# Kernel tuning notes

Measured on AMD Instinct MI355X. Metric: run time of the kernel, lower is better.

Reference implementation:

```python
import jax, jax.numpy as jnp
import numpy as np

B, T, S = 64, 128, 512
E, H = 256, 512
GRU_IN = E + 2 * H  # 1280


def setup_inputs() -> dict:
    key = jax.random.key(0)
    ks = jax.random.split(key, 12)
    sc = 0.02
    return {
        "trg_embed": jax.random.normal(ks[0], (B, T, E), jnp.float32),
        "enc_hidden": jax.random.normal(ks[1], (B, S, 2 * H), jnp.float32),
        "enc_final": jax.random.normal(ks[2], (1, B, 2 * H), jnp.float32),
        "data_mask": jnp.ones((B, 1, S), jnp.int32),
        # attention params
        "W_key": jax.random.normal(ks[3], (H, 2 * H), jnp.float32) * sc,
        "W_query": jax.random.normal(ks[4], (H, H), jnp.float32) * sc,
        "w_energy": jax.random.normal(ks[5], (H,), jnp.float32) * sc,
        # bridge
        "W_bridge": jax.random.normal(ks[6], (H, 2 * H), jnp.float32) * sc,
        "b_bridge": jnp.zeros((H,), jnp.float32),
        # GRU (single layer, batch_first)
        "W_ih": jax.random.normal(ks[7], (3 * H, GRU_IN), jnp.float32) * sc,
        "W_hh": jax.random.normal(ks[8], (3 * H, H), jnp.float32) * sc,
        "b_ih": jnp.zeros((3 * H,), jnp.float32),
        "b_hh": jnp.zeros((3 * H,), jnp.float32),
        # pre_out: Linear(H + 2H + E -> H, bias=False)
        "W_pre": jax.random.normal(ks[9], (H, H + 2 * H + E), jnp.float32) * sc,
    }


def _decode(trg_embed, enc_hidden, enc_final, data_mask,
            W_key, W_query, w_energy, W_bridge, b_bridge,
            W_ih, W_hh, b_ih, b_hh, W_pre):
    # bridge: initial hidden state [B, H]
    h0 = jnp.tanh(enc_final[0] @ W_bridge.T + b_bridge)
    # precompute attention keys [B, S, H]
    proj_key = jnp.einsum('bsk,hk->bsh', enc_hidden, W_key)
    mask = data_mask[:, 0, :] != 0  # [B, S]

    def step(h, x_t):  # h: [B,H], x_t: [B,E]
        # Bahdanau attention
        q = x_t_query = h @ W_query.T                      # [B, H]
        e = jnp.einsum('bsh,h->bs', jnp.tanh(q[:, None, :] + proj_key), w_energy)  # [B,S]
        e = jnp.where(mask, e, -1e9)
        alphas = jax.nn.softmax(e, axis=-1)                # [B, S]
        context = jnp.einsum('bs,bsd->bd', alphas, enc_hidden)  # [B, 2H]
        # GRU cell
        x = jnp.concatenate([x_t, context], axis=-1)       # [B, E+2H]
        gx = x @ W_ih.T + b_ih                             # [B, 3H]
        gh = h @ W_hh.T + b_hh                             # [B, 3H]
        rx, zx, nx = jnp.split(gx, 3, axis=-1)
        rh, zh, nh = jnp.split(gh, 3, axis=-1)
        r = jax.nn.sigmoid(rx + rh)
        z = jax.nn.sigmoid(zx + zh)
        n = jnp.tanh(nx + r * nh)
        h_new = (1.0 - z) * n + z * h                      # [B, H]
        # pre-output projection
        pre = jnp.concatenate([x_t, h_new, context], axis=-1) @ W_pre.T  # [B, H]
        return h_new, (h_new, pre)

    xs = jnp.transpose(trg_embed, (1, 0, 2))  # [T, B, E]
    h_last, (states, pre_outs) = jax.lax.scan(step, h0, xs)
    decoder_states = jnp.transpose(states, (1, 0, 2))      # [B, T, H]
    pre_output_vectors = jnp.transpose(pre_outs, (1, 0, 2))  # [B, T, H]
    hidden = h_last[None]                                  # [1, B, H]
    return decoder_states, hidden, pre_output_vectors


def reference(trg_embed, enc_hidden, enc_final, data_mask,
              W_key, W_query, w_energy, W_bridge, b_bridge,
              W_ih, W_hh, b_ih, b_hh, W_pre):
    return _decode(trg_embed, enc_hidden, enc_final, data_mask,
                   W_key, W_query, w_energy, W_bridge, b_bridge,
                   W_ih, W_hh, b_ih, b_hh, W_pre)
```

## Files before the change

kernel.cpp:

```cpp
#include <hip/hip_runtime.h>


#define LDSS 40

typedef short bf16x8 __attribute__((ext_vector_type(8)));
typedef float f32x4 __attribute__((ext_vector_type(4)));

__device__ inline ushort f2b(float f) {
    unsigned int u = __float_as_uint(f);
    return (ushort)((u + 0x7FFFu + ((u >> 16) & 1u)) >> 16);
}
__device__ inline float b2f(ushort u) {
    return __uint_as_float(((unsigned int)u) << 16);
}
__device__ inline float fast_tanh(float x) {
    x = fminf(fmaxf(x, -15.f), 15.f);
    float ex = __expf(2.f * x);
    return (ex - 1.f) / (ex + 1.f);
}

__global__ void f2b4_kernel(const float4* __restrict__ in, ushort4* __restrict__ out, int n4) {
    int i = blockIdx.x * blockDim.x + threadIdx.x;
    int stride = gridDim.x * blockDim.x;
    for (; i < n4; i += stride) {
        float4 v = in[i];
        ushort4 o;
        o.x = f2b(v.x); o.y = f2b(v.y); o.z = f2b(v.z); o.w = f2b(v.w);
        out[i] = o;
    }
}

template <bool AF32, bool ATOMIC>
__device__ inline void gemm64x64(const void* __restrict__ Av,
                                 const ushort* __restrict__ B,
                                 ushort* As, ushort* Bs,
                                 int lda, int ldb, int kbeg, int kend,
                                 float* Cf, ushort* Cb, long ldc,
                                 long m0, long n0)
{
    const int tid  = threadIdx.x;
    const int wave = tid >> 6;
    const int lane = tid & 63;
    const int row  = tid >> 2;
    const int kcol = (tid & 3) * 8;
    const int lrow = lane & 15;
    const int quad = lane >> 4;

    f32x4 acc[4];
#pragma unroll
    for (int i = 0; i < 4; i++) acc[i] = f32x4{0.f, 0.f, 0.f, 0.f};

    const ushort* Ab  = (const ushort*)Av + (m0 + row) * (long)lda + kcol;
    const float*  Afp = (const float*)Av + (m0 + row) * (long)lda + kcol;
    const ushort* Bp  = B + (n0 + row) * (long)ldb + kcol;
    ushort* AsW = As + row * LDSS + kcol;
    ushort* BsW = Bs + row * LDSS + kcol;
    const ushort* AsR = As + (wave * 16 + lrow) * LDSS + quad * 8;
    const ushort* BsR = Bs + lrow * LDSS + quad * 8;

    for (int k0 = kbeg; k0 < kend; k0 += 32) {
        uint4 av;
        if (AF32) {
            float4 f0 = *(const float4*)(Afp + k0);
            float4 f1 = *(const float4*)(Afp + k0 + 4);
            av.x = (uint)f2b(f0.x) | ((uint)f2b(f0.y) << 16);
            av.y = (uint)f2b(f0.z) | ((uint)f2b(f0.w) << 16);
            av.z = (uint)f2b(f1.x) | ((uint)f2b(f1.y) << 16);
            av.w = (uint)f2b(f1.z) | ((uint)f2b(f1.w) << 16);
        } else {
            av = *(const uint4*)(Ab + k0);
        }
        uint4 bv = *(const uint4*)(Bp + k0);
        __syncthreads();
        *(uint4*)AsW = av;
        *(uint4*)BsW = bv;
        __syncthreads();
        bf16x8 af = *(const bf16x8*)AsR;
#pragma unroll
        for (int nf = 0; nf < 4; nf++) {
            bf16x8 bfv = *(const bf16x8*)(BsR + nf * 16 * LDSS);
            acc[nf] = __builtin_amdgcn_mfma_f32_16x16x32_bf16(af, bfv, acc[nf], 0, 0, 0);
        }
    }

#pragma unroll
    for (int nf = 0; nf < 4; nf++) {
#pragma unroll
        for (int r = 0; r < 4; r++) {
            long m = m0 + wave * 16 + quad * 4 + r;
            long n = n0 + nf * 16 + lrow;
            float v = acc[nf][r];
            if (ATOMIC)      atomicAdd(&Cf[m * ldc + n], v);
            else if (Cf)     Cf[m * ldc + n] = v;
            else             Cb[m * ldc + n] = f2b(v);
        }
    }
}

template <bool AF32>
__global__ void gemm_nt(const void* __restrict__ A, const ushort* __restrict__ B,
                        float* Cf, ushort* Cb,
                        int lda, int ldb, long ldc, int K, int nTilesN)
{
    __shared__ ushort As[64 * LDSS];
    __shared__ ushort Bs[64 * LDSS];
    long m0 = (long)(blockIdx.x / nTilesN) * 64;
    long n0 = (long)(blockIdx.x % nTilesN) * 64;
    gemm64x64<AF32, false>(A, B, As, Bs, lda, ldb, 0, K, Cf, Cb, ldc, m0, n0);
}

__global__ void q_kernel(const ushort* __restrict__ h_b, const ushort* __restrict__ Wq,
                         float* q)
{
    __shared__ ushort As[64 * LDSS];
    __shared__ ushort Bs[64 * LDSS];
    int kc = blockIdx.x >> 3, nt = blockIdx.x & 7;
    gemm64x64<false, true>(h_b, Wq, As, Bs, 512, 512, kc * 256, kc * 256 + 256,
                           q, nullptr, 512, 0, (long)nt * 64);
}

__global__ void gxgh_kernel(const ushort* __restrict__ xcat, const ushort* __restrict__ h_b,
                            const ushort* __restrict__ cat2r,
                            const ushort* __restrict__ Wih, const ushort* __restrict__ Whh,
                            const ushort* __restrict__ Wpre,
                            float* gx, float* gh, float* pre_out, int t)
{
    __shared__ ushort As[64 * LDSS];
    __shared__ ushort Bs[64 * LDSS];
    int bid = blockIdx.x;
    if (bid < 32) {
        if (t == 0) return;
        int kc = bid >> 3, nt = bid & 7;
        gemm64x64<false, true>(cat2r, Wpre, As, Bs, 1792, 1792, kc * 448, kc * 448 + 448,
                               pre_out + (long)(t - 1) * 512, nullptr, 65536, 0, (long)nt * 64);
    } else if (bid < 80) {
        int b3 = bid - 32, kc = b3 / 24, nt = b3 % 24;
        gemm64x64<false, true>(h_b, Whh, As, Bs, 512, 512, kc * 256, kc * 256 + 256,
                               gh, nullptr, 1536, 0, (long)nt * 64);
    } else {
        int b4 = bid - 80, nt = b4 % 24, kc = b4 / 24;
        gemm64x64<false, true>(xcat, Wih, As, Bs, 1280, 1280, kc * 320, kc * 320 + 320,
                               gx, nullptr, 1536, 0, (long)nt * 64);
    }
}

__global__ void e_kernel(const ushort* __restrict__ pk, const float* __restrict__ q,
                         const float* __restrict__ wE, const int* __restrict__ mask,
                         float* __restrict__ e)
{
    int wid  = (blockIdx.x * blockDim.x + threadIdx.x) >> 6;
    int lane = threadIdx.x & 63;
    int b  = wid >> 7;
    int s0 = (wid & 127) << 2;
    const float* qp = q + ((long)b << 9) + lane * 8;
    const float* wp = wE + lane * 8;
    float4 q0 = *(const float4*)qp, q1 = *(const float4*)(qp + 4);
    float4 w0 = *(const float4*)wp, w1 = *(const float4*)(wp + 4);
    const ushort* pkb = pk + (((long)(b << 9) + s0) << 9) + lane * 8;
    bf16x8 pv = *(const bf16x8*)pkb;
#pragma unroll
    for (int j = 0; j < 4; j++) {
        bf16x8 pn;
        if (j < 3) pn = *(const bf16x8*)(pkb + ((long)(j + 1) << 9));
        float acc;
        acc  = fast_tanh(q0.x + b2f((ushort)pv[0])) * w0.x;
        acc += fast_tanh(q0.y + b2f((ushort)pv[1])) * w0.y;
        acc += fast_tanh(q0.z + b2f((ushort)pv[2])) * w0.z;
        acc += fast_tanh(q0.w + b2f((ushort)pv[3])) * w0.w;
        acc += fast_tanh(q1.x + b2f((ushort)pv[4])) * w1.x;
        acc += fast_tanh(q1.y + b2f((ushort)pv[5])) * w1.y;
        acc += fast_tanh(q1.z + b2f((ushort)pv[6])) * w1.z;
        acc += fast_tanh(q1.w + b2f((ushort)pv[7])) * w1.w;
#pragma unroll
        for (int off = 32; off; off >>= 1) acc += __shfl_xor(acc, off);
        if (lane == 0) {
            int i = (b << 9) + s0 + j;
            e[i] = (mask[i] != 0) ? acc : -1e9f;
        }
        pv = pn;
    }
}

__global__ void sc_kernel(const float* __restrict__ e,
                          const float* __restrict__ encf, const ushort* __restrict__ encb,
                          int useb, const float* __restrict__ trg,
                          ushort* __restrict__ xcat, ushort* __restrict__ cat2, int t)
{
    __shared__ float alpha[512];
    __shared__ float red[256];
    __shared__ float part[256];
    int b  = blockIdx.x >> 4;
    int dc = blockIdx.x & 15;
    int tid = threadIdx.x;
    float p0 = __expf(e[(b << 9) + tid]);
    float p1 = __expf(e[(b << 9) + 256 + tid]);
    alpha[tid] = p0;
    alpha[tid + 256] = p1;
    red[tid] = p0 + p1;
    __syncthreads();
    for (int off = 128; off; off >>= 1) {
        if (tid < off) red[tid] += red[tid + off];
        __syncthreads();
    }
    float inv = 1.f / red[0];
    int dl = tid & 63;
    int sr = tid >> 6;
    int d  = (dc << 6) + dl;
    float a0 = 0.f, a1 = 0.f, a2 = 0.f, a3 = 0.f;
    if (useb) {
        const ushort* p = encb + ((long)b << 19) + d;
        for (int s = sr; s < 512; s += 16) {
            a0 += alpha[s]      * b2f(p[(long)s << 10]);
            a1 += alpha[s + 4]  * b2f(p[(long)(s + 4) << 10]);
            a2 += alpha[s + 8]  * b2f(p[(long)(s + 8) << 10]);
            a3 += alpha[s + 12] * b2f(p[(long)(s + 12) << 10]);
        }
    } else {
        const float* p = encf + ((long)b << 19) + d;
        for (int s = sr; s < 512; s += 16) {
            a0 += alpha[s]      * p[(long)s << 10];
            a1 += alpha[s + 4]  * p[(long)(s + 4) << 10];
            a2 += alpha[s + 8]  * p[(long)(s + 8) << 10];
            a3 += alpha[s + 12] * p[(long)(s + 12) << 10];
        }
    }
    part[tid] = ((a0 + a1) + (a2 + a3));
    __syncthreads();
    if (sr == 0) {
        float ctx = (part[dl] + part[64 + dl] + part[128 + dl] + part[192 + dl]) * inv;
        ushort cb = f2b(ctx);
        xcat[b * 1280 + 256 + d] = cb;
        cat2[b * 1792 + 768 + d] = cb;
    } else if (sr == 1 && dc < 4) {
        ushort xv = f2b(trg[((long)b * 128 + t) * 256 + (dc << 6) + dl]);
        xcat[b * 1280 + (dc << 6) + dl] = xv;
        cat2[b * 1792 + (dc << 6) + dl] = xv;
    }
}

__global__ void gates_kernel(float* __restrict__ gx, float* __restrict__ gh,
                             const float* __restrict__ bih, const float* __restrict__ bhh,
                             float* __restrict__ h, ushort* __restrict__ h_b,
                             ushort* __restrict__ cat2, float* __restrict__ d_states,
                             float* __restrict__ q, float* __restrict__ out_pre, int t)
{
    int idx = blockIdx.x * blockDim.x + threadIdx.x;
    int b = idx >> 9, j = idx & 511;
    float* gxp = gx + b * 1536;
    float* ghp = gh + b * 1536;
    float rx = gxp[j]        + bih[j];
    float zx = gxp[j + 512]  + bih[j + 512];
    float nx = gxp[j + 1024] + bih[j + 1024];
    float rh = ghp[j]        + bhh[j];
    float zh = ghp[j + 512]  + bhh[j + 512];
    float nh = ghp[j + 1024] + bhh[j + 1024];
    float r = 1.f / (1.f + __expf(-(rx + rh)));
    float z = 1.f / (1.f + __expf(-(zx + zh)));
    float n = fast_tanh(nx + r * nh);
    float hn = (1.f - z) * n + z * h[idx];
    h[idx] = hn;
    h_b[idx] = f2b(hn);
    cat2[b * 1792 + 256 + j] = f2b(hn);
    d_states[((long)b * 128 + t) * 512 + j] = hn;
    gxp[j] = 0.f; gxp[j + 512] = 0.f; gxp[j + 1024] = 0.f;
    ghp[j] = 0.f; ghp[j + 512] = 0.f; ghp[j + 1024] = 0.f;
    q[idx] = 0.f;
    out_pre[((long)b * 128 + t) * 512 + j] = 0.f;
}

__global__ void btanh_kernel(const float* __restrict__ br, const float* __restrict__ bbr,
                             float* __restrict__ h, ushort* __restrict__ h_b,
                             float* __restrict__ q, float* __restrict__ gh,
                             float* __restrict__ gx)
{
    int idx = blockIdx.x * blockDim.x + threadIdx.x;
    int b = idx >> 9, j = idx & 511;
    float v = fast_tanh(br[idx] + bbr[j]);
    h[idx] = v;
    h_b[idx] = f2b(v);
    q[idx] = 0.f;
    gh[b * 1536 + j] = 0.f; gh[b * 1536 + j + 512] = 0.f; gh[b * 1536 + j + 1024] = 0.f;
    gx[b * 1536 + j] = 0.f; gx[b * 1536 + j + 512] = 0.f; gx[b * 1536 + j + 1024] = 0.f;
}

__global__ void hid_kernel(const float* __restrict__ h, float* __restrict__ out)
{
    int idx = blockIdx.x * blockDim.x + threadIdx.x;
    out[idx] = h[idx];
}

extern "C" void kernel_launch(void* const* d_in, const int* in_sizes, int n_in,
                              void* d_out, int out_size, void* d_ws, size_t ws_size,
                              hipStream_t stream)
{
    (void)in_sizes; (void)n_in; (void)out_size;
    const float* trg  = (const float*)d_in[0];
    const float* enc  = (const float*)d_in[1];
    const float* encF = (const float*)d_in[2];
    const int*   mask = (const int*)d_in[3];
    const float* Wkey = (const float*)d_in[4];
    const float* Wq   = (const float*)d_in[5];
    const float* wE   = (const float*)d_in[6];
    const float* Wbr  = (const float*)d_in[7];
    const float* bbr  = (const float*)d_in[8];
    const float* Wih  = (const float*)d_in[9];
    const float* Whh  = (const float*)d_in[10];
    const float* bih  = (const float*)d_in[11];
    const float* bhh  = (const float*)d_in[12];
    const float* Wpre = (const float*)d_in[13];

    char* p = (char*)d_ws;
    auto alloc = [&](size_t bytes) { void* r = (void*)p; p += (bytes + 255) & ~(size_t)255; return r; };
    ushort* pk     = (ushort*)alloc(16777216ul * 2);
    ushort* Wkey_b = (ushort*)alloc(524288ul * 2);
    ushort* Wq_b   = (ushort*)alloc(262144ul * 2);
    ushort* Wbr_b  = (ushort*)alloc(524288ul * 2);
    ushort* Wih_b  = (ushort*)alloc(1966080ul * 2);
    ushort* Whh_b  = (ushort*)alloc(786432ul * 2);
    ushort* Wpre_b = (ushort*)alloc(917504ul * 2);
    float*  h    = (float*)alloc(32768ul * 4);
    ushort* h_b  = (ushort*)alloc(32768ul * 2);
    float*  br   = (float*)alloc(32768ul * 4);
    float*  q    = (float*)alloc(32768ul * 4);
    float*  gh   = (float*)alloc(98304ul * 4);
    float*  gx   = (float*)alloc(98304ul * 4);
    float*  e    = (float*)alloc(32768ul * 4);
    ushort* xcat = (ushort*)alloc(81920ul * 2);
    ushort* cat2 = (ushort*)alloc(229376ul * 2);
    size_t used = (size_t)(p - (char*)d_ws);
    int useb = (used + 33554432ul * 2 <= ws_size) ? 1 : 0;
    ushort* enc_b = useb ? (ushort*)alloc(33554432ul * 2) : nullptr;

    float* out_states = (float*)d_out;
    float* out_hidden = out_states + 64l * 128 * 512;
    float* out_pre    = out_hidden + 64l * 512;

    f2b4_kernel<<<512, 256, 0, stream>>>((const float4*)Wkey, (ushort4*)Wkey_b, 131072);
    f2b4_kernel<<<256, 256, 0, stream>>>((const float4*)Wq,   (ushort4*)Wq_b,   65536);
    f2b4_kernel<<<512, 256, 0, stream>>>((const float4*)Wbr,  (ushort4*)Wbr_b,  131072);
    f2b4_kernel<<<1920, 256, 0, stream>>>((const float4*)Wih, (ushort4*)Wih_b,  491520);
    f2b4_kernel<<<768, 256, 0, stream>>>((const float4*)Whh,  (ushort4*)Whh_b,  196608);
    f2b4_kernel<<<896, 256, 0, stream>>>((const float4*)Wpre, (ushort4*)Wpre_b, 229376);

    if (useb) {
        f2b4_kernel<<<8192, 256, 0, stream>>>((const float4*)enc, (ushort4*)enc_b, 8388608);
        gemm_nt<false><<<4096, 256, 0, stream>>>(enc_b, Wkey_b, nullptr, pk, 1024, 1024, 512, 1024, 8);
    } else {
        gemm_nt<true><<<4096, 256, 0, stream>>>(enc, Wkey_b, nullptr, pk, 1024, 1024, 512, 1024, 8);
    }
    gemm_nt<true><<<8, 256, 0, stream>>>(encF, Wbr_b, br, nullptr, 1024, 1024, 512, 1024, 8);
    btanh_kernel<<<128, 256, 0, stream>>>(br, bbr, h, h_b, q, gh, gx);

    for (int t = 0; t < 128; t++) {
        ushort* cat2w = cat2 + (size_t)(t & 1) * 114688;
        ushort* cat2r = cat2 + (size_t)((t + 1) & 1) * 114688;
        q_kernel<<<16, 256, 0, stream>>>(h_b, Wq_b, q);
        e_kernel<<<2048, 256, 0, stream>>>(pk, q, wE, mask, e);
        sc_kernel<<<1024, 256, 0, stream>>>(e, enc, enc_b, useb, trg, xcat, cat2w, t);
        gxgh_kernel<<<176, 256, 0, stream>>>(xcat, h_b, cat2r, Wih_b, Whh_b, Wpre_b,
                                             gx, gh, out_pre, t);
        gates_kernel<<<128, 256, 0, stream>>>(gx, gh, bih, bhh, h, h_b, cat2w, out_states,
                                              q, out_pre, t);
    }
    gxgh_kernel<<<32, 256, 0, stream>>>(xcat, h_b, cat2 + 114688, Wih_b, Whh_b, Wpre_b,
                                        gx, gh, out_pre, 128);
    hid_kernel<<<128, 256, 0, stream>>>(h, out_hidden);
}
```

Before: 5.921 ms.

## Fuse query GEMV into gates kernel and double K-split in gate GEMMs

New measurement: 9.086 ms. +53.5%, slower.

```diff
diff --git a/kernel.cpp b/kernel.cpp
--- a/kernel.cpp
+++ b/kernel.cpp
@@ -109,14 +109,27 @@
     gemm64x64<AF32, false>(A, B, As, Bs, lda, ldb, 0, K, Cf, Cb, ldc, m0, n0);
 }
 
-__global__ void q_kernel(const ushort* __restrict__ h_b, const ushort* __restrict__ Wq,
-                         float* q)
-{
-    __shared__ ushort As[64 * LDSS];
-    __shared__ ushort Bs[64 * LDSS];
-    int kc = blockIdx.x >> 3, nt = blockIdx.x & 7;
-    gemm64x64<false, true>(h_b, Wq, As, Bs, 512, 512, kc * 256, kc * 256 + 256,
-                           q, nullptr, 512, 0, (long)nt * 64);
+__device__ inline void qgemv(const ushort* hlds, const ushort* __restrict__ Wq,
+                             float* __restrict__ q, int b)
+{
+    int tid = threadIdx.x;
+    int wave = tid >> 6, lane = tid & 63;
+    bf16x8 hv = *(const bf16x8*)(hlds + lane * 8);
+    float hf[8];
+#pragma unroll
+    for (int i = 0; i < 8; i++) hf[i] = b2f((ushort)hv[i]);
+    const ushort* wb = Wq + ((long)(wave << 6) << 9) + lane * 8;
+#pragma unroll 4
+    for (int i = 0; i < 64; i++) {
+        bf16x8 wv = *(const bf16x8*)(wb + ((long)i << 9));
+        float acc = hf[0]*b2f((ushort)wv[0]) + hf[1]*b2f((ushort)wv[1])
+                  + hf[2]*b2f((ushort)wv[2]) + hf[3]*b2f((ushort)wv[3])
+                  + hf[4]*b2f((ushort)wv[4]) + hf[5]*b2f((ushort)wv[5])
+                  + hf[6]*b2f((ushort)wv[6]) + hf[7]*b2f((ushort)wv[7]);
+#pragma unroll
+        for (int off = 32; off; off >>= 1) acc += __shfl_xor(acc, off);
+        if (lane == 0) q[(b << 9) + (wave << 6) + i] = acc;
+    }
 }
 
 __global__ void gxgh_kernel(const ushort* __restrict__ xcat, const ushort* __restrict__ h_b,
@@ -128,18 +141,18 @@
     __shared__ ushort As[64 * LDSS];
     __shared__ ushort Bs[64 * LDSS];
     int bid = blockIdx.x;
-    if (bid < 32) {
+    if (bid < 64) {
         if (t == 0) return;
         int kc = bid >> 3, nt = bid & 7;
-        gemm64x64<false, true>(cat2r, Wpre, As, Bs, 1792, 1792, kc * 448, kc * 448 + 448,
+        gemm64x64<false, true>(cat2r, Wpre, As, Bs, 1792, 1792, kc * 224, kc * 224 + 224,
                                pre_out + (long)(t - 1) * 512, nullptr, 65536, 0, (long)nt * 64);
-    } else if (bid < 80) {
-        int b3 = bid - 32, kc = b3 / 24, nt = b3 % 24;
-        gemm64x64<false, true>(h_b, Whh, As, Bs, 512, 512, kc * 256, kc * 256 + 256,
+    } else if (bid < 160) {
+        int b3 = bid - 64, kc = b3 / 24, nt = b3 % 24;
+        gemm64x64<false, true>(h_b, Whh, As, Bs, 512, 512, kc * 128, kc * 128 + 128,
                                gh, nullptr, 1536, 0, (long)nt * 64);
     } else {
-        int b4 = bid - 80, nt = b4 % 24, kc = b4 / 24;
-        gemm64x64<false, true>(xcat, Wih, As, Bs, 1280, 1280, kc * 320, kc * 320 + 320,
+        int b4 = bid - 160, nt = b4 % 24, kc = b4 / 24;
+        gemm64x64<false, true>(xcat, Wih, As, Bs, 1280, 1280, kc * 160, kc * 160 + 160,
                                gx, nullptr, 1536, 0, (long)nt * 64);
     }
 }
@@ -238,14 +251,17 @@
     }
 }
 
-__global__ void gates_kernel(float* __restrict__ gx, float* __restrict__ gh,
-                             const float* __restrict__ bih, const float* __restrict__ bhh,
-                             float* __restrict__ h, ushort* __restrict__ h_b,
-                             ushort* __restrict__ cat2, float* __restrict__ d_states,
-                             float* __restrict__ q, float* __restrict__ out_pre, int t)
-{
-    int idx = blockIdx.x * blockDim.x + threadIdx.x;
-    int b = idx >> 9, j = idx & 511;
+__global__ void gatesq_kernel(float* __restrict__ gx, float* __restrict__ gh,
+                              const float* __restrict__ bih, const float* __restrict__ bhh,
+                              float* __restrict__ h, ushort* __restrict__ h_b,
+                              ushort* __restrict__ cat2, float* __restrict__ d_states,
+                              const ushort* __restrict__ Wq, float* __restrict__ q,
+                              float* __restrict__ out_pre, int t)
+{
+    __shared__ ushort hlds[512];
+    int b = blockIdx.x;
+    int j = threadIdx.x;
+    int idx = (b << 9) + j;
     float* gxp = gx + b * 1536;
     float* ghp = gh + b * 1536;
     float rx = gxp[j]        + bih[j];
@@ -259,28 +275,36 @@
     float n = fast_tanh(nx + r * nh);
     float hn = (1.f - z) * n + z * h[idx];
     h[idx] = hn;
-    h_b[idx] = f2b(hn);
-    cat2[b * 1792 + 256 + j] = f2b(hn);
+    ushort hb = f2b(hn);
+    h_b[idx] = hb;
+    hlds[j] = hb;
+    cat2[b * 1792 + 256 + j] = hb;
     d_states[((long)b * 128 + t) * 512 + j] = hn;
     gxp[j] = 0.f; gxp[j + 512] = 0.f; gxp[j + 1024] = 0.f;
     ghp[j] = 0.f; ghp[j + 512] = 0.f; ghp[j + 1024] = 0.f;
-    q[idx] = 0.f;
     out_pre[((long)b * 128 + t) * 512 + j] = 0.f;
-}
-
-__global__ void btanh_kernel(const float* __restrict__ br, const float* __restrict__ bbr,
-                             float* __restrict__ h, ushort* __restrict__ h_b,
-                             float* __restrict__ q, float* __restrict__ gh,
-                             float* __restrict__ gx)
-{
-    int idx = blockIdx.x * blockDim.x + threadIdx.x;
-    int b = idx >> 9, j = idx & 511;
+    __syncthreads();
+    qgemv(hlds, Wq, q, b);
+}
+
+__global__ void btanhq_kernel(const float* __restrict__ br, const float* __restrict__ bbr,
+                              float* __restrict__ h, ushort* __restrict__ h_b,
+                              const ushort* __restrict__ Wq, float* __restrict__ q,
+                              float* __restrict__ gh, float* __restrict__ gx)
+{
+    __shared__ ushort hlds[512];
+    int b = blockIdx.x;
+    int j = threadIdx.x;
+    int idx = (b << 9) + j;
     float v = fast_tanh(br[idx] + bbr[j]);
     h[idx] = v;
-    h_b[idx] = f2b(v);
-    q[idx] = 0.f;
+    ushort hb = f2b(v);
+    h_b[idx] = hb;
+    hlds[j] = hb;
     gh[b * 1536 + j] = 0.f; gh[b * 1536 + j + 512] = 0.f; gh[b * 1536 + j + 1024] = 0.f;
     gx[b * 1536 + j] = 0.f; gx[b * 1536 + j + 512] = 0.f; gx[b * 1536 + j + 1024] = 0.f;
+    __syncthreads();
+    qgemv(hlds, Wq, q, b);
 }
 
 __global__ void hid_kernel(const float* __restrict__ h, float* __restrict__ out)
@@ -349,20 +373,19 @@
         gemm_nt<true><<<4096, 256, 0, stream>>>(enc, Wkey_b, nullptr, pk, 1024, 1024, 512, 1024, 8);
     }
     gemm_nt<true><<<8, 256, 0, stream>>>(encF, Wbr_b, br, nullptr, 1024, 1024, 512, 1024, 8);
-    btanh_kernel<<<128, 256, 0, stream>>>(br, bbr, h, h_b, q, gh, gx);
+    btanhq_kernel<<<64, 512, 0, stream>>>(br, bbr, h, h_b, Wq_b, q, gh, gx);
 
     for (int t = 0; t < 128; t++) {
         ushort* cat2w = cat2 + (size_t)(t & 1) * 114688;
         ushort* cat2r = cat2 + (size_t)((t + 1) & 1) * 114688;
-        q_kernel<<<16, 256, 0, stream>>>(h_b, Wq_b, q);
         e_kernel<<<2048, 256, 0, stream>>>(pk, q, wE, mask, e);
         sc_kernel<<<1024, 256, 0, stream>>>(e, enc, enc_b, useb, trg, xcat, cat2w, t);
-        gxgh_kernel<<<176, 256, 0, stream>>>(xcat, h_b, cat2r, Wih_b, Whh_b, Wpre_b,
+        gxgh_kernel<<<352, 256, 0, stream>>>(xcat, h_b, cat2r, Wih_b, Whh_b, Wpre_b,
                                              gx, gh, out_pre, t);
-        gates_kernel<<<128, 256, 0, stream>>>(gx, gh, bih, bhh, h, h_b, cat2w, out_states,
-                                              q, out_pre, t);
-    }
-    gxgh_kernel<<<32, 256, 0, stream>>>(xcat, h_b, cat2 + 114688, Wih_b, Whh_b, Wpre_b,
+        gatesq_kernel<<<64, 512, 0, stream>>>(gx, gh, bih, bhh, h, h_b, cat2w, out_states,
+                                              Wq_b, q, out_pre, t);
+    }
+    gxgh_kernel<<<64, 256, 0, stream>>>(xcat, h_b, cat2 + 114688, Wih_b, Whh_b, Wpre_b,
                                         gx, gh, out_pre, 128);
     hid_kernel<<<128, 256, 0, stream>>>(h, out_hidden);
 }
```
